# Kernel optimization log

Hardware: AMD Instinct MI355X
Metric: run time of the kernel (lower is better)

Reference implementation:

```python
import jax, jax.numpy as jnp
import numpy as np

# irreps_in  = 64x0e + 64x1o + 64x2e  (dim = 64*(1+3+5) = 576)
# irreps_out = 256x0e + 256x1o + 256x2e (dim = 256*9 = 2304)
MUL_IN = 64
MUL_OUT = 256
LS = (0, 1, 2)
N = 100_000
DIN = MUL_IN * sum(2 * l + 1 for l in LS)   # 576


def setup_inputs() -> dict:
    key = jax.random.key(0)
    k0, k1, k2, k3 = jax.random.split(key, 4)
    x = jax.random.normal(k0, (N, DIN), dtype=jnp.float32)
    # e3nn internal weights init ~ N(0,1); one [mul_in, mul_out] matrix per l
    # (the 1x0e axis of the 'uvw' weight has size 1 and is absorbed)
    W0 = jax.random.normal(k1, (MUL_IN, MUL_OUT), dtype=jnp.float32)
    W1 = jax.random.normal(k2, (MUL_IN, MUL_OUT), dtype=jnp.float32)
    W2 = jax.random.normal(k3, (MUL_IN, MUL_OUT), dtype=jnp.float32)
    return {"x": x, "W0": W0, "W1": W1, "W2": W2}


def reference(x, W0, W1, W2):
    # FullyConnectedTensorProduct(in, '0e', out) with s = ones collapses, per l,
    # to: out_l = einsum('nui,uw->nwi', x_l, W_l) / sqrt(fan_in)
    # where fan_in = mul_in (element path normalization; wigner_3j(l,0,l) =
    # I/sqrt(2l+1) cancels the sqrt(2l+1) component irrep normalization).
    n = x.shape[0]
    scale = np.float32(1.0 / np.sqrt(MUL_IN))
    outs = []
    off = 0
    for l, W in zip(LS, (W0, W1, W2)):
        d = 2 * l + 1
        blk = x[:, off:off + MUL_IN * d].reshape(n, MUL_IN, d)  # [n, u, i]
        off += MUL_IN * d
        o = jnp.einsum('nui,uw->nwi', blk, W) * scale           # [n, w, i]
        outs.append(o.reshape(n, MUL_OUT * d))
    return jnp.concatenate(outs, axis=-1)  # [n, 2304]
```

## Files before the change

kernel.cpp:

```cpp
#include <hip/hip_runtime.h>


typedef __attribute__((ext_vector_type(8))) short bf16x8;
typedef __attribute__((ext_vector_type(4))) float f32x4;

__device__ __forceinline__ unsigned short f2bf(float f) {
  union { float f; unsigned u; } a; a.f = f;
  unsigned r = a.u + 0x7fffu + ((a.u >> 16) & 1u);
  return (unsigned short)(r >> 16);
}

template<int D, int TM, int OFF_IN, int OFF_OUT>
__launch_bounds__(256)
__global__ void tp_kernel(const float* __restrict__ x, const float* __restrict__ W,
                          float* __restrict__ out, int n_total) {
  constexpr int SP       = 72;
  constexpr int MROWS    = TM * D;
  constexpr int RT       = MROWS / 16;
  constexpr int ROWELEMS = 64 * D;
  constexpr int HALF     = 128 * D;
  constexpr int SMEM_A   = MROWS * SP * 2;
  constexpr int SMEM_C   = TM * HALF * 4;
  constexpr int SMEM     = (SMEM_C > SMEM_A) ? SMEM_C : SMEM_A;

  __shared__ __align__(16) char smraw[SMEM];
  unsigned short* sa = (unsigned short*)smraw;
  float*          sc = (float*)smraw;

  const int tid  = threadIdx.x;
  const int wv   = tid >> 6;
  const int lane = tid & 63;
  const int quad = lane >> 4;
  const int nc   = lane & 15;
  const int n0   = blockIdx.x * TM;

  bf16x8 bfrag[4][2];
#pragma unroll
  for (int t = 0; t < 4; ++t) {
#pragma unroll
    for (int s = 0; s < 2; ++s) {
      const int w = wv * 64 + t * 16 + nc;
#pragma unroll
      for (int j = 0; j < 8; ++j) {
        const int u = s * 32 + quad * 8 + j;
        bfrag[t][s][j] = (short)f2bf(W[u * 256 + w]);
      }
    }
  }

  constexpr int STAGE_IT = (TM * ROWELEMS / 4) / 256;
#pragma unroll
  for (int it = 0; it < STAGE_IT; ++it) {
    const int F  = (tid + it * 256) * 4;
    const int ln = F / ROWELEMS;
    const int e  = F % ROWELEMS;
    const int n  = n0 + ln;
    float4 v = make_float4(0.f, 0.f, 0.f, 0.f);
    if (n < n_total) v = *(const float4*)(x + (size_t)n * 576 + OFF_IN + e);
    const float vv[4] = {v.x, v.y, v.z, v.w};
#pragma unroll
    for (int k = 0; k < 4; ++k) {
      const int ek = e + k;
      const int u  = ek / D;
      const int i  = ek % D;
      sa[(ln * D + i) * SP + u] = f2bf(vv[k]);
    }
  }
  __syncthreads();

  f32x4 acc[RT][4];
#pragma unroll
  for (int r = 0; r < RT; ++r)
#pragma unroll
    for (int t = 0; t < 4; ++t)
      acc[r][t] = (f32x4){0.f, 0.f, 0.f, 0.f};

#pragma unroll
  for (int r = 0; r < RT; ++r) {
#pragma unroll
    for (int s = 0; s < 2; ++s) {
      const bf16x8 af = *(const bf16x8*)(sa + (r * 16 + nc) * SP + s * 32 + quad * 8);
#pragma unroll
      for (int t = 0; t < 4; ++t)
        acc[r][t] = __builtin_amdgcn_mfma_f32_16x16x32_bf16(af, bfrag[t][s], acc[r][t], 0, 0, 0);
    }
  }

  constexpr int OUT_IT = (TM * HALF / 4) / 256;
#pragma unroll
  for (int h = 0; h < 2; ++h) {
    __syncthreads();
    if ((wv >> 1) == h) {
#pragma unroll
      for (int r = 0; r < RT; ++r) {
#pragma unroll
        for (int t = 0; t < 4; ++t) {
          const int wl = wv * 64 + t * 16 + nc - h * 128;
#pragma unroll
          for (int reg = 0; reg < 4; ++reg) {
            const int m  = r * 16 + quad * 4 + reg;
            const int ln = m / D;
            const int i  = m % D;
            sc[(ln * 128 + wl) * D + i] = acc[r][t][reg] * 0.125f;
          }
        }
      }
    }
    __syncthreads();
#pragma unroll
    for (int it = 0; it < OUT_IT; ++it) {
      const int F  = (tid + it * 256) * 4;
      const int ln = F / HALF;
      const int p  = F % HALF;
      const int n  = n0 + ln;
      if (n < n_total)
        *(float4*)(out + (size_t)n * 2304 + OFF_OUT + h * HALF + p) = *(const float4*)(sc + F);
    }
  }
}

extern "C" void kernel_launch(void* const* d_in, const int* in_sizes, int n_in,
                              void* d_out, int out_size, void* d_ws, size_t ws_size,
                              hipStream_t stream) {
  const float* x  = (const float*)d_in[0];
  const float* W0 = (const float*)d_in[1];
  const float* W1 = (const float*)d_in[2];
  const float* W2 = (const float*)d_in[3];
  float* out = (float*)d_out;
  const int n = in_sizes[0] / 576;

  tp_kernel<1, 64,   0,    0><<<(n + 63) / 64, 256, 0, stream>>>(x, W0, out, n);
  tp_kernel<3, 16,  64,  256><<<(n + 15) / 16, 256, 0, stream>>>(x, W1, out, n);
  tp_kernel<5, 16, 256, 1024><<<(n + 15) / 16, 256, 0, stream>>>(x, W2, out, n);
}
```

Measured before the change: 1.149 ms.

## Fuse three per-l kernels into one kernel with contiguous row loads

Replaces the three per-irrep launches with one fused kernel. Each block loads full 576-float input rows once, scatters them into a shared bf16 tile covering l=0,1,2, and then runs the MFMA GEMM and output staging for each l in turn. Output is written in four 64-column chunks, one per wave, using nontemporal loads and stores, with launch bounds set for 3 blocks per SM. This removes two kernel launches and gives fully contiguous input reads, at the cost of extra barriers and three weight-fragment reloads per block.

```diff
diff --git a/kernel.cpp b/kernel.cpp
--- a/kernel.cpp
+++ b/kernel.cpp
@@ -10,22 +10,80 @@
   return (unsigned short)(r >> 16);
 }
 
-template<int D, int TM, int OFF_IN, int OFF_OUT>
-__launch_bounds__(256)
-__global__ void tp_kernel(const float* __restrict__ x, const float* __restrict__ W,
-                          float* __restrict__ out, int n_total) {
-  constexpr int SP       = 72;
-  constexpr int MROWS    = TM * D;
-  constexpr int RT       = MROWS / 16;
-  constexpr int ROWELEMS = 64 * D;
-  constexpr int HALF     = 128 * D;
-  constexpr int SMEM_A   = MROWS * SP * 2;
-  constexpr int SMEM_C   = TM * HALF * 4;
-  constexpr int SMEM     = (SMEM_C > SMEM_A) ? SMEM_C : SMEM_A;
+constexpr int SP    = 72;
+constexpr int TM    = 16;
+constexpr int AROWS = TM * 9;
 
-  __shared__ __align__(16) char smraw[SMEM];
-  unsigned short* sa = (unsigned short*)smraw;
-  float*          sc = (float*)smraw;
+template<int D, int AROW0, int OFF_OUT>
+__device__ __forceinline__ void process_l(const float* __restrict__ W,
+                                          const unsigned short* sa, float* sc,
+                                          float* __restrict__ out, int n_total, int n0,
+                                          int tid, int wv, int quad, int nc) {
+  bf16x8 bfrag[4][2];
+#pragma unroll
+  for (int t = 0; t < 4; ++t)
+#pragma unroll
+    for (int s = 0; s < 2; ++s) {
+      const int w = wv * 64 + t * 16 + nc;
+#pragma unroll
+      for (int j = 0; j < 8; ++j)
+        bfrag[t][s][j] = (short)f2bf(W[(s * 32 + quad * 8 + j) * 256 + w]);
+    }
+
+  f32x4 acc[D][4];
+#pragma unroll
+  for (int r = 0; r < D; ++r)
+#pragma unroll
+    for (int t = 0; t < 4; ++t)
+      acc[r][t] = (f32x4){0.f, 0.f, 0.f, 0.f};
+
+#pragma unroll
+  for (int r = 0; r < D; ++r)
+#pragma unroll
+    for (int s = 0; s < 2; ++s) {
+      const bf16x8 af = *(const bf16x8*)(sa + (AROW0 + r * 16 + nc) * SP + s * 32 + quad * 8);
+#pragma unroll
+      for (int t = 0; t < 4; ++t)
+        acc[r][t] = __builtin_amdgcn_mfma_f32_16x16x32_bf16(af, bfrag[t][s], acc[r][t], 0, 0, 0);
+    }
+
+#pragma unroll
+  for (int ch = 0; ch < 4; ++ch) {
+    __syncthreads();
+    if (wv == ch) {
+#pragma unroll
+      for (int r = 0; r < D; ++r)
+#pragma unroll
+        for (int t = 0; t < 4; ++t) {
+          const int wl = t * 16 + nc;
+#pragma unroll
+          for (int reg = 0; reg < 4; ++reg) {
+            const int m = r * 16 + quad * 4 + reg;
+            sc[((m / D) * 64 + wl) * D + (m % D)] = acc[r][t][reg] * 0.125f;
+          }
+        }
+    }
+    __syncthreads();
+#pragma unroll
+    for (int it = 0; it < D; ++it) {
+      const int F  = (tid + it * 256) * 4;
+      const int ln = F / (64 * D);
+      const int p  = F % (64 * D);
+      const int n  = n0 + ln;
+      if (n < n_total)
+        __builtin_nontemporal_store(*(const f32x4*)(sc + F),
+                                    (f32x4*)(out + (size_t)n * 2304 + OFF_OUT + ch * 64 * D + p));
+    }
+  }
+}
+
+__launch_bounds__(256, 3)
+__global__ void tp_fused(const float* __restrict__ x,
+                         const float* __restrict__ W0, const float* __restrict__ W1,
+                         const float* __restrict__ W2,
+                         float* __restrict__ out, int n_total) {
+  __shared__ __align__(16) unsigned short sa[AROWS * SP];
+  __shared__ __align__(16) float sc[TM * 64 * 5];
 
   const int tid  = threadIdx.x;
   const int wv   = tid >> 6;
@@ -34,89 +92,38 @@
   const int nc   = lane & 15;
   const int n0   = blockIdx.x * TM;
 
-  bf16x8 bfrag[4][2];
 #pragma unroll
-  for (int t = 0; t < 4; ++t) {
+  for (int it = 0; it < 9; ++it) {
+    const int F  = (tid + it * 256) * 4;
+    const int ln = F / 576;
+    const int e  = F % 576;
+    const int n  = n0 + ln;
+    f32x4 v = {0.f, 0.f, 0.f, 0.f};
+    if (n < n_total)
+      v = __builtin_nontemporal_load((const f32x4*)(x + (size_t)n * 576 + e));
+    if (e < 64) {
 #pragma unroll
-    for (int s = 0; s < 2; ++s) {
-      const int w = wv * 64 + t * 16 + nc;
+      for (int k = 0; k < 4; ++k)
+        sa[ln * SP + (e + k)] = f2bf(v[k]);
+    } else if (e < 256) {
 #pragma unroll
-      for (int j = 0; j < 8; ++j) {
-        const int u = s * 32 + quad * 8 + j;
-        bfrag[t][s][j] = (short)f2bf(W[u * 256 + w]);
+      for (int k = 0; k < 4; ++k) {
+        const int ee = e - 64 + k;
+        sa[(16 + ln * 3 + (ee % 3)) * SP + (ee / 3)] = f2bf(v[k]);
       }
-    }
-  }
-
-  constexpr int STAGE_IT = (TM * ROWELEMS / 4) / 256;
+    } else {
 #pragma unroll
-  for (int it = 0; it < STAGE_IT; ++it) {
-    const int F  = (tid + it * 256) * 4;
-    const int ln = F / ROWELEMS;
-    const int e  = F % ROWELEMS;
-    const int n  = n0 + ln;
-    float4 v = make_float4(0.f, 0.f, 0.f, 0.f);
-    if (n < n_total) v = *(const float4*)(x + (size_t)n * 576 + OFF_IN + e);
-    const float vv[4] = {v.x, v.y, v.z, v.w};
-#pragma unroll
-    for (int k = 0; k < 4; ++k) {
-      const int ek = e + k;
-      const int u  = ek / D;
-      const int i  = ek % D;
-      sa[(ln * D + i) * SP + u] = f2bf(vv[k]);
+      for (int k = 0; k < 4; ++k) {
+        const int ee = e - 256 + k;
+        sa[(64 + ln * 5 + (ee % 5)) * SP + (ee / 5)] = f2bf(v[k]);
+      }
     }
   }
   __syncthreads();
 
-  f32x4 acc[RT][4];
-#pragma unroll
-  for (int r = 0; r < RT; ++r)
-#pragma unroll
-    for (int t = 0; t < 4; ++t)
-      acc[r][t] = (f32x4){0.f, 0.f, 0.f, 0.f};
-
-#pragma unroll
-  for (int r = 0; r < RT; ++r) {
-#pragma unroll
-    for (int s = 0; s < 2; ++s) {
-      const bf16x8 af = *(const bf16x8*)(sa + (r * 16 + nc) * SP + s * 32 + quad * 8);
-#pragma unroll
-      for (int t = 0; t < 4; ++t)
-        acc[r][t] = __builtin_amdgcn_mfma_f32_16x16x32_bf16(af, bfrag[t][s], acc[r][t], 0, 0, 0);
-    }
-  }
-
-  constexpr int OUT_IT = (TM * HALF / 4) / 256;
-#pragma unroll
-  for (int h = 0; h < 2; ++h) {
-    __syncthreads();
-    if ((wv >> 1) == h) {
-#pragma unroll
-      for (int r = 0; r < RT; ++r) {
-#pragma unroll
-        for (int t = 0; t < 4; ++t) {
-          const int wl = wv * 64 + t * 16 + nc - h * 128;
-#pragma unroll
-          for (int reg = 0; reg < 4; ++reg) {
-            const int m  = r * 16 + quad * 4 + reg;
-            const int ln = m / D;
-            const int i  = m % D;
-            sc[(ln * 128 + wl) * D + i] = acc[r][t][reg] * 0.125f;
-          }
-        }
-      }
-    }
-    __syncthreads();
-#pragma unroll
-    for (int it = 0; it < OUT_IT; ++it) {
-      const int F  = (tid + it * 256) * 4;
-      const int ln = F / HALF;
-      const int p  = F % HALF;
-      const int n  = n0 + ln;
-      if (n < n_total)
-        *(float4*)(out + (size_t)n * 2304 + OFF_OUT + h * HALF + p) = *(const float4*)(sc + F);
-    }
-  }
+  process_l<1,  0,    0>(W0, sa, sc, out, n_total, n0, tid, wv, quad, nc);
+  process_l<3, 16,  256>(W1, sa, sc, out, n_total, n0, tid, wv, quad, nc);
+  process_l<5, 64, 1024>(W2, sa, sc, out, n_total, n0, tid, wv, quad, nc);
 }
 
 extern "C" void kernel_launch(void* const* d_in, const int* in_sizes, int n_in,
@@ -129,7 +136,5 @@
   float* out = (float*)d_out;
   const int n = in_sizes[0] / 576;
 
-  tp_kernel<1, 64,   0,    0><<<(n + 63) / 64, 256, 0, stream>>>(x, W0, out, n);
-  tp_kernel<3, 16,  64,  256><<<(n + 15) / 16, 256, 0, stream>>>(x, W1, out, n);
-  tp_kernel<5, 16, 256, 1024><<<(n + 15) / 16, 256, 0, stream>>>(x, W2, out, n);
+  tp_fused<<<(n + TM - 1) / TM, 256, 0, stream>>>(x, W0, W1, W2, out, n);
 }
```

After: 1.125 ms. 2.0% less time.
